# Kernel optimization log

Hardware: AMD Instinct MI355X
Metric: run time of the kernel (lower is better)

The kernel has to match this reference:

```python
import jax, jax.numpy as jnp
import numpy as np

RATIO = 1.0  # self.ratio from __init__


def setup_inputs() -> dict:
    key = jax.random.key(0)
    ks = jax.random.split(key, 12)
    B, C, N = 128, 2048, 196
    S, L, M = 312, 300, 1024  # attritube_num, w2v_length, med_dim
    inp = {
        "feat": jax.random.normal(ks[0], (B, C, N), dtype=jnp.float32),
        "att_emb": jax.random.normal(ks[1], (S, L), dtype=jnp.float32),
        # Linear params (PyTorch layout: W is [out, in], y = x @ W.T + b)
        "Wq": jax.random.normal(ks[2], (M, L), dtype=jnp.float32) * (1.0 / np.sqrt(L)),
        "bq": jnp.zeros((M,), dtype=jnp.float32),
        "Wk": jax.random.normal(ks[3], (M, C), dtype=jnp.float32) * (1.0 / np.sqrt(C)),
        "bk": jnp.zeros((M,), dtype=jnp.float32),
        "Wv": jax.random.normal(ks[4], (M, C), dtype=jnp.float32) * (1.0 / np.sqrt(C)),
        "bv": jnp.zeros((M,), dtype=jnp.float32),
        "Wo": jax.random.normal(ks[5], (C, M), dtype=jnp.float32) * (1.0 / np.sqrt(M)),
        "bo": jnp.zeros((C,), dtype=jnp.float32),
        "V_final": jax.random.normal(ks[6], (S, C), dtype=jnp.float32),
    }
    return inp


def reference(feat, att_emb, Wq, bq, Wk, bk, Wv, bv, Wo, bo, V_final):
    # feat: [B, C, N], att_emb: [S, L]
    query = att_emb @ Wq.T + bq                      # [S, M]
    feat_t = jnp.swapaxes(feat, 1, 2)                # [B, N, C]
    k = feat_t @ Wk.T + bk                           # [B, N, M]
    v = feat_t @ Wv.T + bv                           # [B, N, M]
    scores = jnp.einsum('sm,bnm->bsn', query, k)     # [B, S, N]
    attn = jax.nn.softmax(scores, axis=-1)           # softmax over N (dim=2)
    attented = jnp.einsum('bsn,bnm->bsm', attn, v)   # [B, S, M]
    attented_o = attented @ Wo.T + bo                # [B, S, C]
    feat_pool = jnp.mean(feat, axis=-1)              # avg_pool1d(kernel=N) -> [B, C]
    final = feat_pool[:, None, :] + RATIO * attented_o  # [B, S, C]
    v2s = jnp.einsum('bsc,sc->bs', final, V_final)   # [B, S]
    return v2s
```

## Files before the change

### kernel.cpp

```cpp
#include <hip/hip_runtime.h>
#include <hip/hip_bf16.h>
#include <cstdint>

typedef _Float16 half_t;
typedef _Float16 f16x8 __attribute__((ext_vector_type(8), aligned(16)));
typedef _Float16 f16x4 __attribute__((ext_vector_type(4), aligned(8)));
typedef _Float16 f16x2 __attribute__((ext_vector_type(2), aligned(4)));
typedef float f32x4 __attribute__((ext_vector_type(4)));

#define B_ 128
#define C_ 2048
#define N_ 196
#define S_ 312
#define L_ 300
#define LP 320
#define M_ 1024
#define NP 224
#define SP 384

__device__ __forceinline__ void gload16(const half_t* g, half_t* l) {
    __builtin_amdgcn_global_load_lds((const __attribute__((address_space(1))) void*)g,
                                     (__attribute__((address_space(3))) void*)l, 16, 0, 0);
}

struct GDesc {
    const half_t* A; const half_t* Bm;
    float* outF; half_t* outH; const float* bias;
    int kdim; int ldo; int rowmul; int rowoff;
};


__device__ __forceinline__ void dev_convert(int c, int t, const float* __restrict__ att,
                                            const float* __restrict__ Wq, const float* __restrict__ V,
                                            const float* __restrict__ Wo, const float* __restrict__ bv,
                                            half_t* __restrict__ atth, half_t* __restrict__ wqh,
                                            half_t* __restrict__ vh, float* __restrict__ Wobv) {
    if (c < 120) {
        size_t e = ((size_t)c * 256 + t) * 4;
        int r = (int)(e / LP), cc = (int)(e % LP);
        f16x4 h;
#pragma unroll
        for (int j = 0; j < 4; ++j) h[j] = (half_t)((r < S_ && cc + j < L_) ? att[(size_t)r * L_ + cc + j] : 0.f);
        *(f16x4*)&atth[e] = h;
    } else if (c < 440) {
        size_t e = ((size_t)(c - 120) * 256 + t) * 4;
        int r = (int)(e / LP), cc = (int)(e % LP);
        f16x4 h;
#pragma unroll
        for (int j = 0; j < 4; ++j) h[j] = (half_t)((cc + j < L_) ? Wq[(size_t)r * L_ + cc + j] : 0.f);
        *(f16x4*)&wqh[e] = h;
    } else if (c < 1208) {
        size_t e = ((size_t)(c - 440) * 256 + t) * 4;
        int r = (int)(e / C_);
        f16x4 h;
        if (r < S_) {
            float4 v = *(const float4*)&V[e];
            h[0] = (half_t)v.x; h[1] = (half_t)v.y; h[2] = (half_t)v.z; h[3] = (half_t)v.w;
        } else {
            h[0] = h[1] = h[2] = h[3] = (half_t)0.f;
        }
        *(f16x4*)&vh[e] = h;
    } else {
        int cc = (c - 1208) * 4 + (t >> 6);
        int lane = t & 63;
        const float* wr_ = Wo + (size_t)cc * M_;
        float acc = 0;
#pragma unroll
        for (int i = 0; i < 16; ++i) acc += wr_[lane + 64 * i] * bv[lane + 64 * i];
        for (int off = 32; off; off >>= 1) acc += __shfl_xor(acc, off);
        if (lane == 0) Wobv[cc] = acc;
    }
}

__device__ __forceinline__ void dev_transp3(int r3, int t, const float* __restrict__ Wk,
                                            const float* __restrict__ Wo, const float* __restrict__ Wv,
                                            half_t* __restrict__ WkT, half_t* __restrict__ WoT,
                                            half_t* __restrict__ WvT, char* smc) {
    half_t (*lsT)[72] = (half_t(*)[72])smc;
    int z = r3 >> 9, r = r3 & 511;
    const float* in; half_t* out; int R, Cc, bx, by;
    if (z == 0)      { in = Wk; out = WkT; R = 1024; Cc = 2048; bx = r & 31; by = r >> 5; }
    else if (z == 1) { in = Wo; out = WoT; R = 2048; Cc = 1024; bx = r & 15; by = r >> 4; }
    else             { in = Wv; out = WvT; R = 1024; Cc = 2048; bx = r & 31; by = r >> 5; }
    int c0 = bx * 64, r0 = by * 64;
#pragma unroll
    for (int i = 0; i < 4; ++i) {
        int Q = t + 256 * i;
        int rq = Q >> 5, cq = Q & 31;
        int rr = 2 * rq, cc = 2 * cq;
        const float* p0 = in + (size_t)(r0 + rr) * Cc + c0 + cc;
        float2 va = *(const float2*)p0;
        float2 vb = *(const float2*)(p0 + Cc);
        f16x2 w0; w0[0] = (half_t)va.x; w0[1] = (half_t)vb.x;
        f16x2 w1; w1[0] = (half_t)va.y; w1[1] = (half_t)vb.y;
        *(f16x2*)&lsT[cc][rr]     = w0;
        *(f16x2*)&lsT[cc + 1][rr] = w1;
    }
    __syncthreads();
    int cl = t >> 2, ch = t & 3;
    f16x8 v0 = *(const f16x8*)&lsT[cl][ch * 16];
    f16x8 v1 = *(const f16x8*)&lsT[cl][ch * 16 + 8];
    half_t* po = out + (size_t)(c0 + cl) * R + r0 + ch * 16;
    *(f16x8*)po = v0;
    *(f16x8*)(po + 8) = v1;
}

__device__ __forceinline__ void dev_transf(const float* __restrict__ feat, half_t* __restrict__ featT,
                                           float* __restrict__ poolp, int nT, int cT, int bb, int t, char* smc) {
    half_t (*lsT)[72] = (half_t(*)[72])smc;
    float* poolLs = (float*)(smc + 64 * 72 * 2);
    int n0 = nT * 64, c0 = cT * 64;
    const float* fb = feat + (size_t)bb * C_ * N_;
#pragma unroll
    for (int i = 0; i < 4; ++i) {
        int Q = t + 256 * i;
        int cq = Q >> 5, nq = Q & 31;
        int cc = 2 * cq, nn = 2 * nq;
        int n = n0 + nn;
        float2 va = {0, 0}, vb = {0, 0};
        if (n < N_) {
            const float* p0 = fb + (size_t)(c0 + cc) * N_ + n;
            va = *(const float2*)p0;
            vb = *(const float2*)(p0 + N_);
        }
        f16x2 w0; w0[0] = (half_t)va.x; w0[1] = (half_t)vb.x;
        f16x2 w1; w1[0] = (half_t)va.y; w1[1] = (half_t)vb.y;
        *(f16x2*)&lsT[nn][cc]     = w0;
        *(f16x2*)&lsT[nn + 1][cc] = w1;
        float sA = va.x + va.y, sB = vb.x + vb.y;
        for (int off = 16; off; off >>= 1) { sA += __shfl_xor(sA, off); sB += __shfl_xor(sB, off); }
        if ((t & 31) == 0) { poolLs[cc] = sA; poolLs[cc + 1] = sB; }
    }
    __syncthreads();
    int nl = t >> 2, ch = t & 3;
    int n = n0 + nl;
    if (n < NP) {
        f16x8 v0 = *(const f16x8*)&lsT[nl][ch * 16];
        f16x8 v1 = *(const f16x8*)&lsT[nl][ch * 16 + 8];
        half_t* po = featT + ((size_t)bb * NP + n) * C_ + c0 + ch * 16;
        *(f16x8*)po = v0;
        *(f16x8*)(po + 8) = v1;
    }
    if (t < 64) poolp[((size_t)nT * B_ + bb) * C_ + c0 + t] = poolLs[t];
}

__device__ __forceinline__ void dev_prep(GDesc d, int bx, int by, int t, char* smc) {
    half_t* lsA = (half_t*)smc;
    half_t* lsB = lsA + 3 * 4096;
    int wid = t >> 6, lane = t & 63;
    const int rA0 = by * 128, rB0 = bx * 128;
    int wr = wid >> 1, wc = wid & 1;
    int g = lane >> 4, l15 = lane & 15;
    const int r_ = t >> 2;
    const int gsrc = ((t & 3) ^ ((t >> 3) & 3)) * 8;
    const int kdim = d.kdim;
    const half_t* pA  = d.A + (size_t)(rA0 + r_) * kdim + gsrc;
    const half_t* pA2 = pA + (size_t)64 * kdim;
    const half_t* pB  = d.Bm + (size_t)(rB0 + r_) * kdim + gsrc;
    const half_t* pB2 = pB + (size_t)64 * kdim;
    const int lo = t * 8;
    const int xsw = ((l15 >> 1) & 3) * 8;
    f32x4 acc[4][4] = {};
    int nk = kdim >> 5;

#define PSTAGE(slot, kc)                                    \
    do {                                                    \
        gload16(pA + (kc), &lsA[(slot) * 4096 + lo]);       \
        gload16(pA2 + (kc), &lsA[(slot) * 4096 + lo + 2048]); \
        gload16(pB + (kc), &lsB[(slot) * 4096 + lo]);       \
        gload16(pB2 + (kc), &lsB[(slot) * 4096 + lo + 2048]); \
    } while (0)

    PSTAGE(0, 0);
    PSTAGE(1, 32);
    int cur = 0, nxt = 2;
    for (int tk = 0; tk < nk; ++tk) {
        if (tk == nk - 1) asm volatile("s_waitcnt vmcnt(0)" ::: "memory");
        else              asm volatile("s_waitcnt vmcnt(4)" ::: "memory");
        __builtin_amdgcn_s_barrier();
        __builtin_amdgcn_sched_barrier(0);
        f16x8 af[4], bf[4];
#pragma unroll
        for (int i = 0; i < 4; ++i) af[i] = *(const f16x8*)&lsA[cur * 4096 + (wr * 64 + i * 16 + l15) * 32 + ((g * 8) ^ xsw)];
#pragma unroll
        for (int j = 0; j < 4; ++j) bf[j] = *(const f16x8*)&lsB[cur * 4096 + (wc * 64 + j * 16 + l15) * 32 + ((g * 8) ^ xsw)];
        if (tk + 2 < nk) PSTAGE(nxt, (tk + 2) * 32);
#pragma unroll
        for (int i = 0; i < 4; ++i)
#pragma unroll
            for (int j = 0; j < 4; ++j)
                acc[i][j] = __builtin_amdgcn_mfma_f32_16x16x32_f16(af[i], bf[j], acc[i][j], 0, 0, 0);
        cur = (cur == 2) ? 0 : cur + 1;
        nxt = (nxt == 2) ? 0 : nxt + 1;
    }
#undef PSTAGE

#pragma unroll
    for (int i = 0; i < 4; ++i) {
        int r0 = rA0 + wr * 64 + i * 16 + g * 4;
#pragma unroll
        for (int j = 0; j < 4; ++j) {
            int c0 = rB0 + wc * 64 + j * 16 + l15;
            float bval = d.bias ? d.bias[c0] : 0.f;
#pragma unroll
            for (int qq = 0; qq < 4; ++qq) {
                int rr = (r0 + qq) * d.rowmul + d.rowoff;
                float val = acc[i][j][qq];
                if (d.outF) d.outF[(size_t)rr * d.ldo + c0] = val;
                if (d.outH) d.outH[(size_t)rr * d.ldo + c0] = (half_t)(val + bval);
            }
        }
    }
}

__device__ __forceinline__ void dev_poolv(const float* __restrict__ poolp, const float* __restrict__ bo,
                                          const float* __restrict__ Wobv, const float* __restrict__ V,
                                          float* __restrict__ base2, int sc, int b, int t, char* smc) {
    float* w = (float*)smc;
    for (int i = t; i < C_; i += 256) {
        float s = poolp[(size_t)b * C_ + i] + poolp[((size_t)B_ + b) * C_ + i] +
                  poolp[((size_t)2 * B_ + b) * C_ + i] + poolp[((size_t)3 * B_ + b) * C_ + i];
        w[i] = s * (1.0f / 196.0f) + bo[i] + Wobv[i];
    }
    __syncthreads();
    int wid = t >> 6, lane = t & 63;
    for (int s = sc * 78 + wid; s < sc * 78 + 78; s += 4) {
        const float* vr = V + (size_t)s * C_;
        float acc = 0;
#pragma unroll
        for (int i = 0; i < 32; ++i) acc += w[lane + 64 * i] * vr[lane + 64 * i];
        for (int off = 32; off; off >>= 1) acc += __shfl_xor(acc, off);
        if (lane == 0) base2[(size_t)b * S_ + s] = acc;
    }
}


__global__ __launch_bounds__(256) void k_d1(const float* __restrict__ feat, const float* __restrict__ att,
                                            const float* __restrict__ Wq, const float* __restrict__ V,
                                            const float* __restrict__ Wo, const float* __restrict__ bv,
                                            const float* __restrict__ Wk, const float* __restrict__ Wv,
                                            half_t* __restrict__ featT, float* __restrict__ poolp,
                                            half_t* __restrict__ atth, half_t* __restrict__ wqh,
                                            half_t* __restrict__ vh, float* __restrict__ Wobv,
                                            half_t* __restrict__ WkT, half_t* __restrict__ WoT,
                                            half_t* __restrict__ WvT) {
    __shared__ __attribute__((aligned(16))) char sm[9472];
    int x = blockIdx.x, t = threadIdx.x;
    if (x < 16384) {
        dev_transf(feat, featT, poolp, x & 3, (x >> 2) & 31, x >> 7, t, sm);
    } else if (x < 16384 + 1720) {
        dev_convert(x - 16384, t, att, Wq, V, Wo, bv, atth, wqh, vh, Wobv);
    } else {
        dev_transp3(x - 16384 - 1720, t, Wk, Wo, Wv, WkT, WoT, WvT, sm);
    }
}

__global__ __launch_bounds__(256) void k_d2(GDesc dq, GDesc dU, const float* __restrict__ poolp,
                                            const float* __restrict__ bo, const float* __restrict__ Wobv,
                                            const float* __restrict__ V, float* __restrict__ base2) {
    __shared__ __attribute__((aligned(16))) char sm[49152];
    int x = blockIdx.x, t = threadIdx.x;
    if (x < 48) {
        dev_prep((x / 24) ? dU : dq, x & 7, (x >> 3) % 3, t, sm);
    } else {
        int r = x - 48;
        dev_poolv(poolp, bo, Wobv, V, base2, r & 3, r >> 2, t, sm);
    }
}

__global__ __launch_bounds__(256) void k_prep2(GDesc d0, GDesc d1) {
    __shared__ __attribute__((aligned(16))) char sm[49152];
    dev_prep(blockIdx.z ? d1 : d0, blockIdx.x, blockIdx.y, threadIdx.x, sm);
}

__global__ __launch_bounds__(256) void k_misc(const float* att, const float* Wq, const float* V,
                                              const float* Wo, const float* bv, const float* Wk,
                                              const float* Wv, half_t* atth, half_t* wqh, half_t* vh,
                                              float* Wobv, half_t* WkT, half_t* WoT, half_t* WvT) {
    __shared__ __attribute__((aligned(16))) char sm[9472];
    int x = blockIdx.x, t = threadIdx.x;
    if (x < 1720) dev_convert(x, t, att, Wq, V, Wo, bv, atth, wqh, vh, Wobv);
    else          dev_transp3(x - 1720, t, Wk, Wo, Wv, WkT, WoT, WvT, sm);
}
__global__ __launch_bounds__(256) void k_transf_only(const float* feat, half_t* featT, float* poolp) {
    __shared__ __attribute__((aligned(16))) char sm[9472];
    dev_transf(feat, featT, poolp, blockIdx.x, blockIdx.y, blockIdx.z, threadIdx.x, sm);
}
__global__ __launch_bounds__(256) void k_poolv_only(const float* poolp, const float* bo, const float* Wobv,
                                                    const float* V, float* base2) {
    __shared__ __attribute__((aligned(16))) char sm[8192];
    dev_poolv(poolp, bo, Wobv, V, base2, blockIdx.x, blockIdx.y, threadIdx.x, sm);
}

__global__ __launch_bounds__(256) void k_fused(const half_t* __restrict__ AstackP, const half_t* __restrict__ featT,
                                               const float* __restrict__ base2, float* __restrict__ out, int b0) {
    __shared__ __attribute__((aligned(16))) half_t lsA[2][192 * 32];
    __shared__ __attribute__((aligned(16))) half_t lsB[3][256 * 32];
    __shared__ float lsE[2][80][4];
    int t = threadIdx.x;
    int bb = blockIdx.x, st = blockIdx.y;
    int wid = t >> 6, lane = t & 63;
    int wr = wid >> 1, wc = wid & 1;
    int g = lane >> 4, l15 = lane & 15;
    const int gsrc = ((t & 3) ^ ((t >> 3) & 3)) * 8;
    const half_t* pA  = AstackP + ((size_t)st * 160 + (t >> 2)) * C_ + gsrc;
    const half_t* pA2 = pA + (size_t)64 * C_;
    const half_t* pA3 = pA + (size_t)128 * C_;
    const half_t* pB  = featT + ((size_t)bb * NP + (t >> 2)) * C_ + gsrc;
    const half_t* pB2 = pB + (size_t)64 * C_;
    const half_t* pB3 = pB + (size_t)128 * C_;
    const half_t* pB4 = pB + (size_t)192 * C_;
    const int lo = t * 8;
    const int xsw = ((l15 >> 1) & 3) * 8;
    f32x4 acc[5][7] = {};

#define FSTAGEA(slot, kc)                            \
    do {                                             \
        gload16(pA + (kc), &lsA[slot][lo]);          \
        gload16(pA2 + (kc), &lsA[slot][lo + 2048]);  \
        gload16(pA3 + (kc), &lsA[slot][lo + 4096]);  \
    } while (0)
#define FSTAGEB(slot, kc)                            \
    do {                                             \
        gload16(pB + (kc), &lsB[slot][lo]);          \
        gload16(pB2 + (kc), &lsB[slot][lo + 2048]);  \
        gload16(pB3 + (kc), &lsB[slot][lo + 4096]);  \
        gload16(pB4 + (kc), &lsB[slot][lo + 6144]);  \
    } while (0)

    FSTAGEA(0, 0);
    FSTAGEB(0, 0);
    FSTAGEB(1, 32);
    for (int tk = 0; tk < 64; ++tk) {
        int ca = tk & 1;
        int cb = tk % 3;
        if (tk == 63) asm volatile("s_waitcnt vmcnt(0)" ::: "memory");
        else          asm volatile("s_waitcnt vmcnt(4)" ::: "memory");
        __builtin_amdgcn_s_barrier();
        __builtin_amdgcn_sched_barrier(0);
        if (tk + 1 < 64) FSTAGEA(ca ^ 1, (tk + 1) * 32);
        if (tk + 2 < 64) FSTAGEB((tk + 2) % 3, (tk + 2) * 32);
        f16x8 af[5], bf[7];
#pragma unroll
        for (int i = 0; i < 5; ++i) af[i] = *(const f16x8*)&lsA[ca][(wr * 80 + i * 16 + l15) * 32 + ((g * 8) ^ xsw)];
#pragma unroll
        for (int j = 0; j < 7; ++j) bf[j] = *(const f16x8*)&lsB[cb][(wc * 112 + j * 16 + l15) * 32 + ((g * 8) ^ xsw)];
        asm volatile("s_waitcnt lgkmcnt(0)" ::: "memory");
        __builtin_amdgcn_sched_barrier(0);
#pragma unroll
        for (int i = 0; i < 5; ++i)
#pragma unroll
            for (int j = 0; j < 7; ++j)
                acc[i][j] = __builtin_amdgcn_mfma_f32_16x16x32_f16(af[i], bf[j], acc[i][j], 0, 0, 0);
    }
#undef FSTAGEA
#undef FSTAGEB

#pragma unroll
    for (int i = 0; i < 5; ++i) {
#pragma unroll
        for (int pair = 0; pair < 2; ++pair) {
            float m = -3.0e38f;
#pragma unroll
            for (int j = 0; j < 7; ++j) {
                int col = wc * 112 + j * 16 + l15;
                if (col < N_) m = fmaxf(m, acc[i][j][2 * pair]);
            }
#pragma unroll
            for (int off = 1; off < 16; off <<= 1) m = fmaxf(m, __shfl_xor(m, off));
            float ls = 0.f, dt = 0.f;
#pragma unroll
            for (int j = 0; j < 7; ++j) {
                int col = wc * 112 + j * 16 + l15;
                if (col < N_) {
                    float p = __expf(acc[i][j][2 * pair] - m);
                    ls += p;
                    dt += p * acc[i][j][2 * pair + 1];
                }
            }
#pragma unroll
            for (int off = 1; off < 16; off <<= 1) { ls += __shfl_xor(ls, off); dt += __shfl_xor(dt, off); }
            if (l15 == 0) {
                int pr = wr * 40 + i * 8 + g * 2 + pair;
                lsE[wc][pr][0] = m; lsE[wc][pr][1] = ls; lsE[wc][pr][2] = dt;
            }
        }
    }
    __syncthreads();
    if (t < 80) {
        float m0 = lsE[0][t][0], l0 = lsE[0][t][1], dv0 = lsE[0][t][2];
        float m1 = lsE[1][t][0], l1 = lsE[1][t][1], dv1 = lsE[1][t][2];
        float M = fmaxf(m0, m1);
        float e0 = __expf(m0 - M), e1 = __expf(m1 - M);
        float L = l0 * e0 + l1 * e1, D = dv0 * e0 + dv1 * e1;
        int s = st * 80 + t;
        if (s < S_) {
            int bg = b0 + bb;
            out[(size_t)bg * S_ + s] = base2[(size_t)bg * S_ + s] + D / L;
        }
    }
}

extern "C" void kernel_launch(void* const* d_in, const int* in_sizes, int n_in,
                              void* d_out, int out_size, void* d_ws, size_t ws_size,
                              hipStream_t stream) {
    const float* feat = (const float*)d_in[0];
    const float* att  = (const float*)d_in[1];
    const float* Wq   = (const float*)d_in[2];
    const float* bq   = (const float*)d_in[3];
    const float* Wk   = (const float*)d_in[4];
    const float* Wv   = (const float*)d_in[6];
    const float* bv   = (const float*)d_in[7];
    const float* Wo   = (const float*)d_in[8];
    const float* bo   = (const float*)d_in[9];
    const float* V    = (const float*)d_in[10];
    float* out = (float*)d_out;

    auto AL = [](size_t x) { return (x + 255) & ~(size_t)255; };
    const size_t szAstk = (size_t)768 * C_ * 2;
    const size_t szQh   = (size_t)SP * M_ * 2;
    const size_t szVh   = (size_t)SP * C_ * 2;
    const size_t szUh   = (size_t)SP * M_ * 2;
    const size_t szWT   = (size_t)C_ * M_ * 2;
    const size_t szAtth = (size_t)SP * LP * 2;
    const size_t szWqh  = (size_t)M_ * LP * 2;
    const size_t szPoolp = (size_t)4 * B_ * C_ * 4;
    const size_t szBase = (size_t)B_ * S_ * 4;
    const size_t szWobv = (size_t)C_ * 4;
    size_t fixed = AL(szAstk) + AL(szQh) + AL(szVh) + AL(szUh) + 3 * AL(szWT) +
                   AL(szAtth) + AL(szWqh) + AL(szPoolp) + AL(szBase) + AL(szWobv);

    int nsplit = 1;
    while (nsplit < 32) {
        size_t nB = B_ / nsplit;
        size_t need = fixed + AL(nB * NP * C_ * 2 + 131072);
        if (need <= ws_size) break;
        nsplit *= 2;
    }
    int nB = B_ / nsplit;

    char* p = (char*)d_ws;
    half_t* AstackP = (half_t*)p; p += AL(szAstk);
    half_t* qh     = (half_t*)p; p += AL(szQh);
    half_t* Vh     = (half_t*)p; p += AL(szVh);
    half_t* Uh     = (half_t*)p; p += AL(szUh);
    half_t* WkT    = (half_t*)p; p += AL(szWT);
    half_t* WoT    = (half_t*)p; p += AL(szWT);
    half_t* WvT    = (half_t*)p; p += AL(szWT);
    half_t* atth   = (half_t*)p; p += AL(szAtth);
    half_t* wqh    = (half_t*)p; p += AL(szWqh);
    float*  poolp  = (float*)p;  p += AL(szPoolp);
    float*  base2  = (float*)p;  p += AL(szBase);
    float*  Wobv   = (float*)p;  p += AL(szWobv);
    half_t* featT  = (half_t*)p;

    GDesc dq{atth, wqh, nullptr, qh, bq, LP, M_, 1, 0};
    GDesc dU{Vh, WoT, nullptr, Uh, nullptr, C_, M_, 1, 0};
    GDesc dk{qh, WkT, nullptr, AstackP, nullptr, M_, C_, 2, 0};
    GDesc dv{Uh, WvT, nullptr, AstackP, nullptr, M_, C_, 2, 1};

    if (nsplit == 1) {
        k_d1<<<dim3(16384 + 1720 + 1536), 256, 0, stream>>>(feat, att, Wq, V, Wo, bv, Wk, Wv,
                                                            featT, poolp, atth, wqh, Vh, Wobv,
                                                            WkT, WoT, WvT);
        k_d2<<<dim3(560), 256, 0, stream>>>(dq, dU, poolp, bo, Wobv, V, base2);
        k_prep2<<<dim3(16, 3, 2), 256, 0, stream>>>(dk, dv);
        k_fused<<<dim3(B_, 4), 256, 0, stream>>>(AstackP, featT, base2, out, 0);
    } else {
        k_misc<<<dim3(1720 + 1536), 256, 0, stream>>>(att, Wq, V, Wo, bv, Wk, Wv,
                                                      atth, wqh, Vh, Wobv, WkT, WoT, WvT);
        k_prep2<<<dim3(8, 3, 2), 256, 0, stream>>>(dq, dU);
        k_prep2<<<dim3(16, 3, 2), 256, 0, stream>>>(dk, dv);
        for (int h = 0; h < nsplit; ++h) {
            const float* fh = feat + (size_t)h * nB * C_ * N_;
            k_transf_only<<<dim3(4, 32, nB), 256, 0, stream>>>(fh, featT, poolp);
            k_poolv_only<<<dim3(4, nB), 256, 0, stream>>>(poolp, bo, Wobv, V, base2 + (size_t)h * nB * S_);
            k_fused<<<dim3(nB, 4), 256, 0, stream>>>(AstackP, featT, base2, out, h * nB);
        }
    }
}
```

Before: 218.1 us.

## Widen feat transpose tiles, swizzle LDS, remap fused grid, raise MFMA priority

The feat transpose/convert stage now handles 64x128 tiles per block. It uses float4 global loads and an XOR-swizzled LDS layout with a 272-byte row stride to avoid bank conflicts, which halves the number of transpose blocks and doubles LDS use per block. The fused attention kernel switches to a 1D grid with a remapped block-to-(batch, stripe) assignment so that groups of 8 batches share the same stripe, aimed at better cache locality for the shared weight stack. It also wraps the MFMA loop in s_setprio to favour the math waves. The larger shared-memory footprint may reduce occupancy in the transpose kernel.

```diff
diff --git a/kernel.cpp b/kernel.cpp
--- a/kernel.cpp
+++ b/kernel.cpp
@@ -107,41 +107,59 @@
 
 __device__ __forceinline__ void dev_transf(const float* __restrict__ feat, half_t* __restrict__ featT,
                                            float* __restrict__ poolp, int nT, int cT, int bb, int t, char* smc) {
-    half_t (*lsT)[72] = (half_t(*)[72])smc;
-    float* poolLs = (float*)(smc + 64 * 72 * 2);
-    int n0 = nT * 64, c0 = cT * 64;
+    char* lsTb = smc;
+    float* poolLs = (float*)(smc + 64 * 272);
+    int n0 = nT * 64, c0 = cT * 128;
     const float* fb = feat + (size_t)bb * C_ * N_;
+    const int nq = t & 15, nn = 4 * nq;
+    const int n = n0 + nn;
+    const int key = (nq & 7) << 4;
+    float4 va[4], vb[4];
 #pragma unroll
     for (int i = 0; i < 4; ++i) {
-        int Q = t + 256 * i;
-        int cq = Q >> 5, nq = Q & 31;
-        int cc = 2 * cq, nn = 2 * nq;
-        int n = n0 + nn;
-        float2 va = {0, 0}, vb = {0, 0};
+        int cq = (t >> 4) + 16 * i;
+        va[i] = make_float4(0, 0, 0, 0); vb[i] = make_float4(0, 0, 0, 0);
         if (n < N_) {
-            const float* p0 = fb + (size_t)(c0 + cc) * N_ + n;
-            va = *(const float2*)p0;
-            vb = *(const float2*)(p0 + N_);
+            const float* p0 = fb + (size_t)(c0 + 2 * cq) * N_ + n;
+            va[i] = *(const float4*)p0;
+            vb[i] = *(const float4*)(p0 + N_);
         }
-        f16x2 w0; w0[0] = (half_t)va.x; w0[1] = (half_t)vb.x;
-        f16x2 w1; w1[0] = (half_t)va.y; w1[1] = (half_t)vb.y;
-        *(f16x2*)&lsT[nn][cc]     = w0;
-        *(f16x2*)&lsT[nn + 1][cc] = w1;
-        float sA = va.x + va.y, sB = vb.x + vb.y;
-        for (int off = 16; off; off >>= 1) { sA += __shfl_xor(sA, off); sB += __shfl_xor(sB, off); }
-        if ((t & 31) == 0) { poolLs[cc] = sA; poolLs[cc + 1] = sB; }
+    }
+#pragma unroll
+    for (int i = 0; i < 4; ++i) {
+        int cq = (t >> 4) + 16 * i;
+        char* base = lsTb + (size_t)nn * 272 + ((4 * cq) ^ key);
+        f16x2 w0; w0[0] = (half_t)va[i].x; w0[1] = (half_t)vb[i].x;
+        f16x2 w1; w1[0] = (half_t)va[i].y; w1[1] = (half_t)vb[i].y;
+        f16x2 w2; w2[0] = (half_t)va[i].z; w2[1] = (half_t)vb[i].z;
+        f16x2 w3; w3[0] = (half_t)va[i].w; w3[1] = (half_t)vb[i].w;
+        *(f16x2*)(base)       = w0;
+        *(f16x2*)(base + 272) = w1;
+        *(f16x2*)(base + 544) = w2;
+        *(f16x2*)(base + 816) = w3;
+        float sA = va[i].x + va[i].y + va[i].z + va[i].w;
+        float sB = vb[i].x + vb[i].y + vb[i].z + vb[i].w;
+#pragma unroll
+        for (int off = 1; off < 16; off <<= 1) { sA += __shfl_xor(sA, off); sB += __shfl_xor(sB, off); }
+        if (nq == 0) { int cc = 2 * cq; poolLs[cc] = sA; poolLs[cc + 1] = sB; }
     }
     __syncthreads();
     int nl = t >> 2, ch = t & 3;
-    int n = n0 + nl;
-    if (n < NP) {
-        f16x8 v0 = *(const f16x8*)&lsT[nl][ch * 16];
-        f16x8 v1 = *(const f16x8*)&lsT[nl][ch * 16 + 8];
-        half_t* po = featT + ((size_t)bb * NP + n) * C_ + c0 + ch * 16;
+    int no = n0 + nl;
+    if (no < NP) {
+        int rkey = ((nl >> 2) & 7) << 4;
+        const char* rb = lsTb + (size_t)nl * 272;
+        f16x8 v0 = *(const f16x8*)(rb + ((64 * ch) ^ rkey));
+        f16x8 v1 = *(const f16x8*)(rb + ((64 * ch + 16) ^ rkey));
+        f16x8 v2 = *(const f16x8*)(rb + ((64 * ch + 32) ^ rkey));
+        f16x8 v3 = *(const f16x8*)(rb + ((64 * ch + 48) ^ rkey));
+        half_t* po = featT + ((size_t)bb * NP + no) * C_ + c0 + ch * 32;
         *(f16x8*)po = v0;
         *(f16x8*)(po + 8) = v1;
-    }
-    if (t < 64) poolp[((size_t)nT * B_ + bb) * C_ + c0 + t] = poolLs[t];
+        *(f16x8*)(po + 16) = v2;
+        *(f16x8*)(po + 24) = v3;
+    }
+    if (t < 128) poolp[((size_t)nT * B_ + bb) * C_ + c0 + t] = poolLs[t];
 }
 
 __device__ __forceinline__ void dev_prep(GDesc d, int bx, int by, int t, char* smc) {
@@ -244,14 +262,14 @@
                                             half_t* __restrict__ vh, float* __restrict__ Wobv,
                                             half_t* __restrict__ WkT, half_t* __restrict__ WoT,
                                             half_t* __restrict__ WvT) {
-    __shared__ __attribute__((aligned(16))) char sm[9472];
+    __shared__ __attribute__((aligned(16))) char sm[18176];
     int x = blockIdx.x, t = threadIdx.x;
-    if (x < 16384) {
-        dev_transf(feat, featT, poolp, x & 3, (x >> 2) & 31, x >> 7, t, sm);
-    } else if (x < 16384 + 1720) {
-        dev_convert(x - 16384, t, att, Wq, V, Wo, bv, atth, wqh, vh, Wobv);
+    if (x < 8192) {
+        dev_transf(feat, featT, poolp, x & 3, (x >> 2) & 15, x >> 6, t, sm);
+    } else if (x < 8192 + 1720) {
+        dev_convert(x - 8192, t, att, Wq, V, Wo, bv, atth, wqh, vh, Wobv);
     } else {
-        dev_transp3(x - 16384 - 1720, t, Wk, Wo, Wv, WkT, WoT, WvT, sm);
+        dev_transp3(x - 8192 - 1720, t, Wk, Wo, Wv, WkT, WoT, WvT, sm);
     }
 }
 
@@ -283,7 +301,7 @@
     else          dev_transp3(x - 1720, t, Wk, Wo, Wv, WkT, WoT, WvT, sm);
 }
 __global__ __launch_bounds__(256) void k_transf_only(const float* feat, half_t* featT, float* poolp) {
-    __shared__ __attribute__((aligned(16))) char sm[9472];
+    __shared__ __attribute__((aligned(16))) char sm[18176];
     dev_transf(feat, featT, poolp, blockIdx.x, blockIdx.y, blockIdx.z, threadIdx.x, sm);
 }
 __global__ __launch_bounds__(256) void k_poolv_only(const float* poolp, const float* bo, const float* Wobv,
@@ -298,7 +316,15 @@
     __shared__ __attribute__((aligned(16))) half_t lsB[3][256 * 32];
     __shared__ float lsE[2][80][4];
     int t = threadIdx.x;
-    int bb = blockIdx.x, st = blockIdx.y;
+    int nB = gridDim.x >> 2;
+    int bb, st;
+    if ((nB & 7) == 0) {
+        bb = ((blockIdx.x >> 5) << 3) + (blockIdx.x & 7);
+        st = (blockIdx.x >> 3) & 3;
+    } else {
+        bb = blockIdx.x >> 2;
+        st = blockIdx.x & 3;
+    }
     int wid = t >> 6, lane = t & 63;
     int wr = wid >> 1, wc = wid & 1;
     int g = lane >> 4, l15 = lane & 15;
@@ -347,11 +373,13 @@
         for (int j = 0; j < 7; ++j) bf[j] = *(const f16x8*)&lsB[cb][(wc * 112 + j * 16 + l15) * 32 + ((g * 8) ^ xsw)];
         asm volatile("s_waitcnt lgkmcnt(0)" ::: "memory");
         __builtin_amdgcn_sched_barrier(0);
+        __builtin_amdgcn_s_setprio(1);
 #pragma unroll
         for (int i = 0; i < 5; ++i)
 #pragma unroll
             for (int j = 0; j < 7; ++j)
                 acc[i][j] = __builtin_amdgcn_mfma_f32_16x16x32_f16(af[i], bf[j], acc[i][j], 0, 0, 0);
+        __builtin_amdgcn_s_setprio(0);
     }
 #undef FSTAGEA
 #undef FSTAGEB
@@ -460,12 +488,12 @@
     GDesc dv{Uh, WvT, nullptr, AstackP, nullptr, M_, C_, 2, 1};
 
     if (nsplit == 1) {
-        k_d1<<<dim3(16384 + 1720 + 1536), 256, 0, stream>>>(feat, att, Wq, V, Wo, bv, Wk, Wv,
-                                                            featT, poolp, atth, wqh, Vh, Wobv,
-                                                            WkT, WoT, WvT);
+        k_d1<<<dim3(8192 + 1720 + 1536), 256, 0, stream>>>(feat, att, Wq, V, Wo, bv, Wk, Wv,
+                                                           featT, poolp, atth, wqh, Vh, Wobv,
+                                                           WkT, WoT, WvT);
         k_d2<<<dim3(560), 256, 0, stream>>>(dq, dU, poolp, bo, Wobv, V, base2);
         k_prep2<<<dim3(16, 3, 2), 256, 0, stream>>>(dk, dv);
-        k_fused<<<dim3(B_, 4), 256, 0, stream>>>(AstackP, featT, base2, out, 0);
+        k_fused<<<dim3(B_ * 4), 256, 0, stream>>>(AstackP, featT, base2, out, 0);
     } else {
         k_misc<<<dim3(1720 + 1536), 256, 0, stream>>>(att, Wq, V, Wo, bv, Wk, Wv,
                                                       atth, wqh, Vh, Wobv, WkT, WoT, WvT);
@@ -473,9 +501,9 @@
         k_prep2<<<dim3(16, 3, 2), 256, 0, stream>>>(dk, dv);
         for (int h = 0; h < nsplit; ++h) {
             const float* fh = feat + (size_t)h * nB * C_ * N_;
-            k_transf_only<<<dim3(4, 32, nB), 256, 0, stream>>>(fh, featT, poolp);
+            k_transf_only<<<dim3(4, 16, nB), 256, 0, stream>>>(fh, featT, poolp);
             k_poolv_only<<<dim3(4, nB), 256, 0, stream>>>(poolp, bo, Wobv, V, base2 + (size_t)h * nB * S_);
-            k_fused<<<dim3(nB, 4), 256, 0, stream>>>(AstackP, featT, base2, out, h * nB);
+            k_fused<<<dim3(nB * 4), 256, 0, stream>>>(AstackP, featT, base2, out, h * nB);
         }
     }
 }
```

After: 287.5 us. 1.32x slower.
